# Kernel optimization log

Measured on AMD Instinct MI355X. Metric: run time of the kernel, lower is better.

The kernel has to match this reference:

```python
import jax, jax.numpy as jnp
import numpy as np

N_FILTRATIONS = 24
TEMPERATURE = 0.15
H1_WEIGHT = 0.5
LAMBDA_TOPO = 0.1


def setup_inputs() -> dict:
    key = jax.random.key(0)
    embeddings = jax.random.normal(key, (4096, 512), dtype=jnp.float32)
    return {"embeddings": embeddings, "step": 0}


def _landscape_loss(embeddings):
    N = embeddings.shape[0]
    emb = embeddings.astype(jnp.float32)
    # pairwise euclidean distances (torch.cdist p=2), safe sqrt for grad at 0
    sq = jnp.sum(emb * emb, axis=1)
    d2 = sq[:, None] + sq[None, :] - 2.0 * (emb @ emb.T)
    d2 = jnp.maximum(d2, 0.0)
    pos = d2 > 1e-12
    dist = jnp.where(pos, jnp.sqrt(jnp.where(pos, d2, 1.0)), 0.0)
    eye = jnp.eye(N, dtype=jnp.float32)
    dist = dist + eye * 1e9  # [N, N], diag pushed to 'infinity'
    off = dist < 1e8
    # thresholds come from .item() in torch -> no grad through them
    d_min = jax.lax.stop_gradient(jnp.min(jnp.where(off, dist, jnp.inf)))
    d_max = jax.lax.stop_gradient(
        jnp.maximum(jnp.max(jnp.where(off, dist, -jnp.inf)), d_min + 1e-4))
    thresholds = jnp.linspace(d_min, d_max, N_FILTRATIONS)

    one_minus_eye = 1.0 - eye

    def step_fn(carry, thresh):
        adj = jax.nn.sigmoid((thresh - dist) / TEMPERATURE) * one_minus_eye
        deg = jnp.clip(jnp.sum(adj, axis=-1), 1e-6, None)
        n_isolated = jnp.sum((deg < 0.5).astype(jnp.float32))  # H0 proxy
        n_edges_soft = jnp.sum(adj) / 2.0
        n_excess = jax.nn.relu(n_edges_soft - (N - 1)) / N  # H1 proxy
        return carry, (n_isolated, n_excess)

    _, (h0, h1) = jax.lax.scan(step_fn, None, thresholds)
    h0_loss = jnp.mean(h0[-8:])
    h1_loss = jnp.mean(h1)
    total = h0_loss + H1_WEIGHT * h1_loss
    return total * LAMBDA_TOPO


def reference(embeddings, step) -> jnp.ndarray:
    # warmup_steps = 0, so the warmup skip branch never triggers;
    # N == max_points, so no subsampling.
    return _landscape_loss(embeddings)
```

## Files before the change

kernel.cpp:

```cpp
#include <hip/hip_runtime.h>
#include <stdint.h>

typedef float f32x4 __attribute__((ext_vector_type(4)));
typedef short s16x8 __attribute__((ext_vector_type(8)));
typedef unsigned short us4 __attribute__((ext_vector_type(4)));

#define NPTS 4096
#define DDIM 512
#define NF   24
#define NBLK 32
#define NB   2048

#define OFF_SQ  4194304
#define OFF_MM  4210688
#define OFF_DEG 4210752
#define OFF_D   4603968
#define OFF_H   38158400ULL
#define WS_A    54935616ULL

static __device__ __forceinline__ ushort f2h(float x) {
    _Float16 h = (_Float16)x;
    return __builtin_bit_cast(unsigned short, h);
}
static __device__ __forceinline__ float h2f(ushort u) {
    return (float)__builtin_bit_cast(_Float16, u);
}

__global__ __launch_bounds__(256) void k_init(float* __restrict__ deg,
                                              unsigned* __restrict__ mm) {
    int i = blockIdx.x * 256 + threadIdx.x;
    if (i < NPTS * NF) deg[i] = 0.0f;
    if (i == 0) { mm[0] = 0x7F7FFFFFu; mm[1] = 0u; }
}

__global__ __launch_bounds__(256) void k_convert(const float* __restrict__ in,
                                                 ushort* __restrict__ Eb,
                                                 float* __restrict__ sq) {
    const int w = threadIdx.x >> 6, lane = threadIdx.x & 63;
    const int row = blockIdx.x * 4 + w;
    const float* src = in + (size_t)row * DDIM + lane * 8;
    float4 a = ((const float4*)src)[0];
    float4 b = ((const float4*)src)[1];
    float v[8] = {a.x, a.y, a.z, a.w, b.x, b.y, b.z, b.w};
    unsigned u[8];
    float ss = 0.0f;
#pragma unroll
    for (int i = 0; i < 8; ++i) {
        ss += v[i] * v[i];
        unsigned bits = __float_as_uint(v[i]);
        u[i] = (bits + 0x7FFFu + ((bits >> 16) & 1u)) >> 16;
    }
    uint4 pk;
    pk.x = u[0] | (u[1] << 16);
    pk.y = u[2] | (u[3] << 16);
    pk.z = u[4] | (u[5] << 16);
    pk.w = u[6] | (u[7] << 16);
    *(uint4*)(Eb + (size_t)row * DDIM + lane * 8) = pk;
#pragma unroll
    for (int s = 1; s < 64; s <<= 1) ss += __shfl_xor(ss, s);
    if (lane == 0) sq[row] = ss;
}

__global__ __launch_bounds__(256) void k_gram128T(const ushort* __restrict__ Eb,
                                                  const float* __restrict__ sq,
                                                  unsigned* __restrict__ mm,
                                                  ushort* __restrict__ D2h) {
    __shared__ ushort SM[4 * 128 * 40];
    __shared__ float sqr[128], sqc[128], red[8];
    const int tid = threadIdx.x;
    const int w = tid >> 6, lane = tid & 63, g = lane >> 4, l15 = lane & 15;

    int bid = blockIdx.x, rb = 0, pre = 0;
    while (pre + (NBLK - rb) <= bid) { pre += NBLK - rb; ++rb; }
    const int cb = rb + (bid - pre);

    if (tid < 128) sqr[tid] = sq[rb * 128 + tid];
    else           sqc[tid - 128] = sq[cb * 128 + (tid - 128)];

    f32x4 acc[2][8];
#pragma unroll
    for (int bi = 0; bi < 2; ++bi)
#pragma unroll
        for (int bj = 0; bj < 8; ++bj) acc[bi][bj] = (f32x4){0.f, 0.f, 0.f, 0.f};

    const int srow0 = tid >> 2, srow1 = 64 + (tid >> 2), sch = tid & 3;
    const size_t aoff0 = (size_t)(rb * 128 + srow0) * DDIM + sch * 8;
    const size_t aoff1 = (size_t)(rb * 128 + srow1) * DDIM + sch * 8;
    const size_t boff0 = (size_t)(cb * 128 + srow0) * DDIM + sch * 8;
    const size_t boff1 = (size_t)(cb * 128 + srow1) * DDIM + sch * 8;

    uint4 ra0 = *(const uint4*)(Eb + aoff0);
    uint4 ra1 = *(const uint4*)(Eb + aoff1);
    uint4 qb0 = *(const uint4*)(Eb + boff0);
    uint4 qb1 = *(const uint4*)(Eb + boff1);
    {
        ushort* A0 = SM;             ushort* B0 = SM + 2 * 5120;
        *(uint4*)(A0 + srow0 * 40 + sch * 8) = ra0;
        *(uint4*)(A0 + srow1 * 40 + sch * 8) = ra1;
        *(uint4*)(B0 + srow0 * 40 + sch * 8) = qb0;
        *(uint4*)(B0 + srow1 * 40 + sch * 8) = qb1;
    }
    int cur = 0;
#pragma unroll 1
    for (int kk = 0; kk < 16; ++kk) {
        if (kk < 15) {
            const int k1 = (kk + 1) * 32;
            ra0 = *(const uint4*)(Eb + aoff0 + k1);
            ra1 = *(const uint4*)(Eb + aoff1 + k1);
            qb0 = *(const uint4*)(Eb + boff0 + k1);
            qb1 = *(const uint4*)(Eb + boff1 + k1);
        }
        __syncthreads();
        const ushort* Ac = SM + cur * 5120;
        const ushort* Bc = SM + 2 * 5120 + cur * 5120;
        s16x8 rf0 = *(const s16x8*)(Ac + (w * 32 + l15) * 40 + g * 8);
        s16x8 rf1 = *(const s16x8*)(Ac + (w * 32 + 16 + l15) * 40 + g * 8);
#pragma unroll
        for (int bj = 0; bj < 8; ++bj) {
            s16x8 cf = *(const s16x8*)(Bc + (bj * 16 + l15) * 40 + g * 8);
            acc[0][bj] = __builtin_amdgcn_mfma_f32_16x16x32_bf16(cf, rf0, acc[0][bj], 0, 0, 0);
            acc[1][bj] = __builtin_amdgcn_mfma_f32_16x16x32_bf16(cf, rf1, acc[1][bj], 0, 0, 0);
        }
        if (kk < 15) {
            ushort* An = SM + (cur ^ 1) * 5120;
            ushort* Bn = SM + 2 * 5120 + (cur ^ 1) * 5120;
            *(uint4*)(An + srow0 * 40 + sch * 8) = ra0;
            *(uint4*)(An + srow1 * 40 + sch * 8) = ra1;
            *(uint4*)(Bn + srow0 * 40 + sch * 8) = qb0;
            *(uint4*)(Bn + srow1 * 40 + sch * 8) = qb1;
        }
        cur ^= 1;
    }
    __syncthreads();

    ushort* T = SM;
    float mn = 3.4e38f, mx = 0.0f;
#pragma unroll
    for (int bi = 0; bi < 2; ++bi) {
        const int trow = rb * 128 + w * 32 + bi * 16 + l15;
        const float srv = sqr[w * 32 + bi * 16 + l15];
#pragma unroll
        for (int bj = 0; bj < 8; ++bj) {
            const int c0 = bj * 16 + g * 4;
            const int tc0 = cb * 128 + c0;
            ushort h[4];
#pragma unroll
            for (int m = 0; m < 4; ++m) {
                float d2 = srv + sqc[c0 + m] - 2.0f * acc[bi][bj][m];
                d2 = fmaxf(d2, 0.0f);
                bool diag = (tc0 + m == trow);
                mn = diag ? mn : fminf(mn, d2);
                mx = diag ? mx : fmaxf(mx, d2);
                h[m] = f2h(diag ? 6.0e4f : d2);
            }
            us4 pk4 = {h[0], h[1], h[2], h[3]};
            *(us4*)(T + (w * 32 + bi * 16 + l15) * 136 + c0) = pk4;
        }
    }
#pragma unroll
    for (int s = 1; s < 64; s <<= 1) {
        mn = fminf(mn, __shfl_xor(mn, s));
        mx = fmaxf(mx, __shfl_xor(mx, s));
    }
    if (lane == 0) { red[w] = mn; red[4 + w] = mx; }
    __syncthreads();
    if (tid == 0) {
        mn = fminf(fminf(red[0], red[1]), fminf(red[2], red[3]));
        mx = fmaxf(fmaxf(red[4], red[5]), fmaxf(red[6], red[7]));
        atomicMin(&mm[0], __float_as_uint(mn));
        atomicMax(&mm[1], __float_as_uint(mx));
    }
    const int orow = tid >> 1, oh = tid & 1;
#pragma unroll
    for (int j = 0; j < 8; ++j) {
        uint4 v = *(const uint4*)(T + orow * 136 + oh * 64 + j * 8);
        *(uint4*)(D2h + (size_t)(rb * 128 + orow) * NPTS + cb * 128 + oh * 64 + j * 8) = v;
    }
    if (rb != cb) {
        const int ocol = tid >> 1;
#pragma unroll
        for (int j2 = 0; j2 < 8; ++j2) {
            unsigned pw[4];
#pragma unroll
            for (int p = 0; p < 4; ++p) {
                unsigned lo = T[(oh * 64 + j2 * 8 + 2 * p) * 136 + ocol];
                unsigned hi = T[(oh * 64 + j2 * 8 + 2 * p + 1) * 136 + ocol];
                pw[p] = lo | (hi << 16);
            }
            *(uint4*)(D2h + (size_t)(cb * 128 + ocol) * NPTS + rb * 128 + oh * 64 + j2 * 8) =
                *(uint4*)pw;
        }
    }
}

__global__ __launch_bounds__(256) void k_hist(const ushort* __restrict__ D2h,
                                              const unsigned* __restrict__ mm,
                                              ushort* __restrict__ H) {
    __shared__ unsigned hist[NB];
    const int tid = threadIdx.x;
    const int row = blockIdx.x;
    for (int i = tid; i < NB; i += 256) hist[i] = 0u;
    const float d2min = __uint_as_float(mm[0]);
    const float d2max = __uint_as_float(mm[1]);
    const float sc = (float)NB / fmaxf(d2max - d2min, 1e-6f);
    __syncthreads();
    const uint4* Dv = (const uint4*)(D2h + (size_t)row * NPTS);
#pragma unroll
    for (int c = 0; c < 2; ++c) {
        uint4 pk = Dv[c * 256 + tid];
        unsigned pw[4] = {pk.x, pk.y, pk.z, pk.w};
#pragma unroll
        for (int i = 0; i < 4; ++i) {
            float a = h2f((ushort)(pw[i] & 0xFFFFu));
            float b = h2f((ushort)(pw[i] >> 16));
            if (a < 3.0e4f) {
                int ba = (int)fminf(fmaxf((a - d2min) * sc, 0.0f), (float)(NB - 1));
                atomicAdd(&hist[ba], 1u);
            }
            if (b < 3.0e4f) {
                int bb = (int)fminf(fmaxf((b - d2min) * sc, 0.0f), (float)(NB - 1));
                atomicAdd(&hist[bb], 1u);
            }
        }
    }
    __syncthreads();
    unsigned o[4];
#pragma unroll
    for (int p = 0; p < 4; ++p) {
        unsigned lo = hist[tid * 8 + 2 * p], hi = hist[tid * 8 + 2 * p + 1];
        o[p] = (lo & 0xFFFFu) | (hi << 16);
    }
    *(uint4*)(H + (size_t)row * NB + tid * 8) = *(uint4*)o;
}

__global__ __launch_bounds__(512) void k_dot(const ushort* __restrict__ H,
                                             const unsigned* __restrict__ mm,
                                             float* __restrict__ deg) {
    __shared__ float Wl[4][NB];
    const int tid = threadIdx.x;
    const int wid = tid >> 6, lane = tid & 63;
    const int row = blockIdx.x * 8 + wid;

    const float d2min = __uint_as_float(mm[0]);
    const float d2max = __uint_as_float(mm[1]);
    const float bw    = fmaxf(d2max - d2min, 1e-6f) / (float)NB;
    const float d_min = d2min > 1e-12f ? sqrtf(d2min) : 0.0f;
    const float d_mx  = d2max > 1e-12f ? sqrtf(d2max) : 0.0f;
    const float d_max = fmaxf(d_mx, d_min + 1e-4f);
    const float stp   = (d_max - d_min) / 23.0f;
    const float S2L   = (1.0f / 0.15f) * 1.44269504f;
    const float Ds2   = stp * S2L;
    const float R     = exp2f(-Ds2);
    const float LIM   = 1073741824.0f;

    float hv[32];
    const ushort* Hr = H + (size_t)row * NB;
#pragma unroll
    for (int j = 0; j < 8; ++j) {
        uint2 pk = *(const uint2*)(Hr + j * 256 + lane * 4);
        hv[j * 4 + 0] = (float)(pk.x & 0xFFFFu);
        hv[j * 4 + 1] = (float)(pk.x >> 16);
        hv[j * 4 + 2] = (float)(pk.y & 0xFFFFu);
        hv[j * 4 + 3] = (float)(pk.y >> 16);
    }

    float e4[4];
#pragma unroll
    for (int q = 0; q < 4; ++q) {
        const int b = tid * 4 + q;
        const float d2c = d2min + ((float)b + 0.5f) * bw;
        const float db = sqrtf(fmaxf(d2c, 0.0f));
        e4[q] = exp2f(fminf((db - d_min) * S2L, 125.0f));
    }

#pragma unroll 1
    for (int ph = 0; ph < 6; ++ph) {
        __syncthreads();
#pragma unroll
        for (int k = 0; k < 4; ++k) {
            f32x4 sg;
#pragma unroll
            for (int q = 0; q < 4; ++q) {
                sg[q] = __builtin_amdgcn_rcpf(1.0f + fminf(e4[q], LIM));
                e4[q] *= R;
            }
            *(f32x4*)(&Wl[k][tid * 4]) = sg;
        }
        __syncthreads();
        float dacc[4];
#pragma unroll
        for (int k = 0; k < 4; ++k) {
            const float* Wr = &Wl[k][0];
            float s = 0.0f;
#pragma unroll
            for (int j = 0; j < 8; ++j) {
                const f32x4 wv = *(const f32x4*)(Wr + j * 256 + lane * 4);
                s += hv[j*4+0]*wv[0] + hv[j*4+1]*wv[1] + hv[j*4+2]*wv[2] + hv[j*4+3]*wv[3];
            }
            dacc[k] = s;
        }
#pragma unroll
        for (int k = 0; k < 4; ++k)
#pragma unroll
            for (int o = 1; o < 64; o <<= 1) dacc[k] += __shfl_xor(dacc[k], o);
        if (lane == 0) {
#pragma unroll
            for (int k = 0; k < 4; ++k) deg[(size_t)row * NF + ph * 4 + k] = dacc[k];
        }
    }
}

__device__ __forceinline__ void gram_tile(const ushort* __restrict__ Eb, int rb, int cb,
                                          ushort* As, ushort* Bs, f32x4 acc[2][8]) {
    const int tid = threadIdx.x;
    const int w = tid >> 6, lane = tid & 63, g = lane >> 4, l15 = lane & 15;
#pragma unroll 1
    for (int kk = 0; kk < DDIM / 32; ++kk) {
        const int k0 = kk * 32;
        __syncthreads();
#pragma unroll
        for (int it = 0; it < 2; ++it) {
            int li  = it * 256 + tid;
            int row = li >> 2, ch = li & 3;
            uint4 va = *(const uint4*)(Eb + (size_t)(rb * 128 + row) * DDIM + k0 + ch * 8);
            uint4 vb = *(const uint4*)(Eb + (size_t)(cb * 128 + row) * DDIM + k0 + ch * 8);
            *(uint4*)(As + row * 32 + ch * 8) = va;
            *(uint4*)(Bs + row * 32 + ch * 8) = vb;
        }
        __syncthreads();
        s16x8 rf0 = *(const s16x8*)(As + (w * 32 + 0 * 16 + l15) * 32 + g * 8);
        s16x8 rf1 = *(const s16x8*)(As + (w * 32 + 1 * 16 + l15) * 32 + g * 8);
#pragma unroll
        for (int bj = 0; bj < 8; ++bj) {
            s16x8 cf = *(const s16x8*)(Bs + (bj * 16 + l15) * 32 + g * 8);
            acc[0][bj] = __builtin_amdgcn_mfma_f32_16x16x32_bf16(cf, rf0, acc[0][bj], 0, 0, 0);
            acc[1][bj] = __builtin_amdgcn_mfma_f32_16x16x32_bf16(cf, rf1, acc[1][bj], 0, 0, 0);
        }
    }
}

__global__ __launch_bounds__(256) void k_minmax(const ushort* __restrict__ Eb,
                                                const float* __restrict__ sq,
                                                unsigned* __restrict__ mm) {
    const int rb = blockIdx.y, cb = blockIdx.x;
    if (cb < rb) return;
    __shared__ ushort As[128 * 32], Bs[128 * 32];
    __shared__ float sqr[128], sqc[128];
    __shared__ float red[8];
    const int tid = threadIdx.x;
    if (tid < 128) sqr[tid] = sq[rb * 128 + tid];
    else           sqc[tid - 128] = sq[cb * 128 + (tid - 128)];
    f32x4 acc[2][8];
#pragma unroll
    for (int bi = 0; bi < 2; ++bi)
#pragma unroll
        for (int bj = 0; bj < 8; ++bj) acc[bi][bj] = (f32x4){0.f, 0.f, 0.f, 0.f};
    gram_tile(Eb, rb, cb, As, Bs, acc);
    const int w = tid >> 6, lane = tid & 63, g = lane >> 4, l15 = lane & 15;
    const float sr0 = sqr[w * 32 + l15], sr1 = sqr[w * 32 + 16 + l15];
    float mn = 3.4e38f, mx = 0.0f;
#pragma unroll
    for (int bi = 0; bi < 2; ++bi)
#pragma unroll
        for (int bj = 0; bj < 8; ++bj)
#pragma unroll
            for (int m = 0; m < 4; ++m) {
                int tr = w * 32 + bi * 16 + l15;
                int tc = bj * 16 + g * 4 + m;
                float d2 = (bi ? sr1 : sr0) + sqc[tc] - 2.0f * acc[bi][bj][m];
                d2 = fmaxf(d2, 0.0f);
                bool diag = (rb == cb) && (tr == tc);
                mn = diag ? mn : fminf(mn, d2);
                mx = diag ? mx : fmaxf(mx, d2);
            }
#pragma unroll
    for (int s = 1; s < 64; s <<= 1) {
        mn = fminf(mn, __shfl_xor(mn, s));
        mx = fmaxf(mx, __shfl_xor(mx, s));
    }
    if (lane == 0) { red[w] = mn; red[4 + w] = mx; }
    __syncthreads();
    if (tid == 0) {
        mn = fminf(fminf(red[0], red[1]), fminf(red[2], red[3]));
        mx = fmaxf(fmaxf(red[4], red[5]), fmaxf(red[6], red[7]));
        atomicMin(&mm[0], __float_as_uint(mn));
        atomicMax(&mm[1], __float_as_uint(mx));
    }
}

__global__ __launch_bounds__(256) void k_accum2(const ushort* __restrict__ Eb,
                                                const float* __restrict__ sq,
                                                const unsigned* __restrict__ mm,
                                                float* __restrict__ deg) {
    const int rb = blockIdx.y, cb = blockIdx.x;
    __shared__ ushort As[128 * 32], Bs[128 * 32];
    __shared__ float sqr[128], sqc[128];
    __shared__ float degr[128][NF];
    const int tid = threadIdx.x;
    if (tid < 128) sqr[tid] = sq[rb * 128 + tid];
    else           sqc[tid - 128] = sq[cb * 128 + (tid - 128)];
    for (int i = tid; i < 128 * NF; i += 256) ((float*)degr)[i] = 0.0f;
    f32x4 acc[2][8];
#pragma unroll
    for (int bi = 0; bi < 2; ++bi)
#pragma unroll
        for (int bj = 0; bj < 8; ++bj) acc[bi][bj] = (f32x4){0.f, 0.f, 0.f, 0.f};
    gram_tile(Eb, rb, cb, As, Bs, acc);
    const int w = tid >> 6, lane = tid & 63, g = lane >> 4, l15 = lane & 15;

    const float dmin2 = __uint_as_float(mm[0]);
    const float dmax2 = __uint_as_float(mm[1]);
    const float d_min = dmin2 > 1e-12f ? sqrtf(dmin2) : 0.0f;
    const float d_mx  = dmax2 > 1e-12f ? sqrtf(dmax2) : 0.0f;
    const float d_max = fmaxf(d_mx, d_min + 1e-4f);
    const float stp   = (d_max - d_min) / 23.0f;
    const float S2L   = (1.0f / 0.15f) * 1.44269504f;
    const float Ds2   = stp * S2L;
    const float R     = exp2f(-Ds2);
    const float LIM   = 1073741824.0f;
    const float ECAP  = 125.0f;

    const float sr0 = sqr[w * 32 + l15], sr1 = sqr[w * 32 + 16 + l15];
    f32x4 ee[2][8];
#pragma unroll
    for (int bi = 0; bi < 2; ++bi)
#pragma unroll
        for (int bj = 0; bj < 8; ++bj)
#pragma unroll
            for (int m = 0; m < 4; ++m) {
                int tr = w * 32 + bi * 16 + l15;
                int tc = bj * 16 + g * 4 + m;
                float d2 = (bi ? sr1 : sr0) + sqc[tc] - 2.0f * acc[bi][bj][m];
                d2 = fmaxf(d2, 0.0f);
                float d = d2 > 1e-12f ? sqrtf(d2) : 0.0f;
                if (rb == cb && tr == tc) d = 1e9f;
                ee[bi][bj][m] = exp2f(fminf((d - d_min) * S2L, ECAP));
            }

#pragma unroll 1
    for (int t = 0; t < NF; ++t) {
        float rs0 = 0.0f, rs1 = 0.0f;
#pragma unroll
        for (int bj = 0; bj < 8; ++bj) {
            {
                f32x4 q = ee[0][bj];
                float A  = 1.0f + fminf(q.x, LIM), B  = 1.0f + fminf(q.y, LIM);
                float Cq = 1.0f + fminf(q.z, LIM), Dq = 1.0f + fminf(q.w, LIM);
                float sAB = A + B,  sCD = Cq + Dq;
                float pAB = A * B,  pCD = Cq * Dq;
                rs0 += (sAB * pCD + sCD * pAB) * __builtin_amdgcn_rcpf(pAB * pCD);
                ee[0][bj] = q * R;
            }
            {
                f32x4 q = ee[1][bj];
                float A  = 1.0f + fminf(q.x, LIM), B  = 1.0f + fminf(q.y, LIM);
                float Cq = 1.0f + fminf(q.z, LIM), Dq = 1.0f + fminf(q.w, LIM);
                float sAB = A + B,  sCD = Cq + Dq;
                float pAB = A * B,  pCD = Cq * Dq;
                rs1 += (sAB * pCD + sCD * pAB) * __builtin_amdgcn_rcpf(pAB * pCD);
                ee[1][bj] = q * R;
            }
        }
        rs0 += __shfl_xor(rs0, 16); rs0 += __shfl_xor(rs0, 32);
        rs1 += __shfl_xor(rs1, 16); rs1 += __shfl_xor(rs1, 32);
        if (g == 0) {
            degr[w * 32 + l15][t]      += rs0;
            degr[w * 32 + 16 + l15][t] += rs1;
        }
    }
    __syncthreads();
    for (int i = tid; i < 128 * NF; i += 256) {
        int r = i / NF, t = i % NF;
        atomicAdd(&deg[(size_t)(rb * 128 + r) * NF + t], degr[r][t]);
    }
}

__global__ __launch_bounds__(256) void k_final(const float* __restrict__ deg,
                                               float* __restrict__ out) {
    const int tid = threadIdx.x;
    float s[NF], cnt[8];
#pragma unroll
    for (int t = 0; t < NF; ++t) s[t] = 0.0f;
#pragma unroll
    for (int k = 0; k < 8; ++k) cnt[k] = 0.0f;
    for (int i = tid; i < NPTS; i += 256) {
        const float* row = deg + (size_t)i * NF;
#pragma unroll
        for (int t = 0; t < NF; ++t) {
            float v = row[t];
            s[t] += v;
            if (t >= 16) cnt[t - 16] += (v < 0.5f) ? 1.0f : 0.0f;
        }
    }
#pragma unroll
    for (int t = 0; t < NF; ++t)
#pragma unroll
        for (int o = 1; o < 64; o <<= 1) s[t] += __shfl_xor(s[t], o);
#pragma unroll
    for (int k = 0; k < 8; ++k)
#pragma unroll
        for (int o = 1; o < 64; o <<= 1) cnt[k] += __shfl_xor(cnt[k], o);
    __shared__ float red[4][32];
    const int w = tid >> 6, lane = tid & 63;
    if (lane == 0) {
#pragma unroll
        for (int t = 0; t < NF; ++t) red[w][t] = s[t];
#pragma unroll
        for (int k = 0; k < 8; ++k) red[w][NF + k] = cnt[k];
    }
    __syncthreads();
    if (tid == 0) {
        float h0 = 0.0f, h1 = 0.0f;
#pragma unroll
        for (int t = 0; t < NF; ++t) {
            float S = red[0][t] + red[1][t] + red[2][t] + red[3][t];
            float edges = S * 0.5f;
            h1 += fmaxf(edges - (float)(NPTS - 1), 0.0f) / (float)NPTS;
        }
#pragma unroll
        for (int k = 0; k < 8; ++k)
            h0 += red[0][NF + k] + red[1][NF + k] + red[2][NF + k] + red[3][NF + k];
        h0 *= (1.0f / 8.0f);
        h1 *= (1.0f / 24.0f);
        out[0] = (h0 + 0.5f * h1) * 0.1f;
    }
}

extern "C" void kernel_launch(void* const* d_in, const int* in_sizes, int n_in,
                              void* d_out, int out_size, void* d_ws, size_t ws_size,
                              hipStream_t stream) {
    (void)in_sizes; (void)n_in; (void)out_size;
    const float* emb = (const float*)d_in[0];
    uint8_t* ws = (uint8_t*)d_ws;
    ushort*   Eb  = (ushort*)(ws);
    float*    sqv = (float*)(ws + OFF_SQ);
    unsigned* mm  = (unsigned*)(ws + OFF_MM);
    float*    deg = (float*)(ws + OFF_DEG);
    ushort*   D2h = (ushort*)(ws + OFF_D);
    ushort*   H   = (ushort*)(ws + OFF_H);
    float*    out = (float*)d_out;
    const bool bigws = (ws_size >= WS_A);

    k_init   <<<dim3(384),      dim3(256), 0, stream>>>(deg, mm);
    k_convert<<<dim3(NPTS / 4), dim3(256), 0, stream>>>(emb, Eb, sqv);
    if (bigws) {
        k_gram128T<<<dim3(NBLK * (NBLK + 1) / 2), dim3(256), 0, stream>>>(Eb, sqv, mm, D2h);
        k_hist    <<<dim3(NPTS),                  dim3(256), 0, stream>>>(D2h, mm, H);
        k_dot     <<<dim3(NPTS / 8),              dim3(512), 0, stream>>>(H, mm, deg);
    } else {
        k_minmax<<<dim3(32, 32), dim3(256), 0, stream>>>(Eb, sqv, mm);
        k_accum2<<<dim3(32, 32), dim3(256), 0, stream>>>(Eb, sqv, mm, deg);
    }
    k_final<<<1, 256, 0, stream>>>(deg, out);
}
```

Measured before the change: 92.42 us.

## Compute full Gram grid with 2x2 warp tiling and fuse degree reduction into k_dot

The symmetric upper-triangle Gram kernel with a transposed write-back is replaced by a full 32x32 block grid, remapped so neighbouring blocks spread across the grid. Each warp now computes a 64x64 sub-tile through a 2x2 warp arrangement, which improves fragment reuse. The uncoalesced transposed stores go away, at the cost of doing twice the MFMA work. k_dot now reduces degrees per block and atomically accumulates the edge sums and isolated counts into a small buffer, so a lighter final kernel replaces the per-row degree array read.

Result: slower. 96.93 us (+4.9%).

```diff
diff --git a/kernel.cpp b/kernel.cpp
--- a/kernel.cpp
+++ b/kernel.cpp
@@ -61,27 +61,27 @@
     if (lane == 0) sq[row] = ss;
 }
 
-__global__ __launch_bounds__(256) void k_gram128T(const ushort* __restrict__ Eb,
-                                                  const float* __restrict__ sq,
-                                                  unsigned* __restrict__ mm,
-                                                  ushort* __restrict__ D2h) {
+__global__ __launch_bounds__(256) void k_gram_full(const ushort* __restrict__ Eb,
+                                                   const float* __restrict__ sq,
+                                                   unsigned* __restrict__ mm,
+                                                   ushort* __restrict__ D2h) {
     __shared__ ushort SM[4 * 128 * 40];
     __shared__ float sqr[128], sqc[128], red[8];
     const int tid = threadIdx.x;
     const int w = tid >> 6, lane = tid & 63, g = lane >> 4, l15 = lane & 15;
-
-    int bid = blockIdx.x, rb = 0, pre = 0;
-    while (pre + (NBLK - rb) <= bid) { pre += NBLK - rb; ++rb; }
-    const int cb = rb + (bid - pre);
+    const int wr = w >> 1, wc = w & 1;
+
+    const int bid = (blockIdx.x & 7) * 128 + (blockIdx.x >> 3);
+    const int rb = bid >> 5, cb = bid & 31;
 
     if (tid < 128) sqr[tid] = sq[rb * 128 + tid];
     else           sqc[tid - 128] = sq[cb * 128 + (tid - 128)];
 
-    f32x4 acc[2][8];
-#pragma unroll
-    for (int bi = 0; bi < 2; ++bi)
-#pragma unroll
-        for (int bj = 0; bj < 8; ++bj) acc[bi][bj] = (f32x4){0.f, 0.f, 0.f, 0.f};
+    f32x4 acc[4][4];
+#pragma unroll
+    for (int i = 0; i < 4; ++i)
+#pragma unroll
+        for (int j = 0; j < 4; ++j) acc[i][j] = (f32x4){0.f, 0.f, 0.f, 0.f};
 
     const int srow0 = tid >> 2, srow1 = 64 + (tid >> 2), sch = tid & 3;
     const size_t aoff0 = (size_t)(rb * 128 + srow0) * DDIM + sch * 8;
@@ -113,14 +113,18 @@
         __syncthreads();
         const ushort* Ac = SM + cur * 5120;
         const ushort* Bc = SM + 2 * 5120 + cur * 5120;
-        s16x8 rf0 = *(const s16x8*)(Ac + (w * 32 + l15) * 40 + g * 8);
-        s16x8 rf1 = *(const s16x8*)(Ac + (w * 32 + 16 + l15) * 40 + g * 8);
-#pragma unroll
-        for (int bj = 0; bj < 8; ++bj) {
-            s16x8 cf = *(const s16x8*)(Bc + (bj * 16 + l15) * 40 + g * 8);
-            acc[0][bj] = __builtin_amdgcn_mfma_f32_16x16x32_bf16(cf, rf0, acc[0][bj], 0, 0, 0);
-            acc[1][bj] = __builtin_amdgcn_mfma_f32_16x16x32_bf16(cf, rf1, acc[1][bj], 0, 0, 0);
-        }
+        s16x8 rf[4], cf[4];
+#pragma unroll
+        for (int i = 0; i < 4; ++i)
+            rf[i] = *(const s16x8*)(Ac + (wr * 64 + i * 16 + l15) * 40 + g * 8);
+#pragma unroll
+        for (int j = 0; j < 4; ++j)
+            cf[j] = *(const s16x8*)(Bc + (wc * 64 + j * 16 + l15) * 40 + g * 8);
+#pragma unroll
+        for (int i = 0; i < 4; ++i)
+#pragma unroll
+            for (int j = 0; j < 4; ++j)
+                acc[i][j] = __builtin_amdgcn_mfma_f32_16x16x32_bf16(cf[j], rf[i], acc[i][j], 0, 0, 0);
         if (kk < 15) {
             ushort* An = SM + (cur ^ 1) * 5120;
             ushort* Bn = SM + 2 * 5120 + (cur ^ 1) * 5120;
@@ -136,17 +140,18 @@
     ushort* T = SM;
     float mn = 3.4e38f, mx = 0.0f;
 #pragma unroll
-    for (int bi = 0; bi < 2; ++bi) {
-        const int trow = rb * 128 + w * 32 + bi * 16 + l15;
-        const float srv = sqr[w * 32 + bi * 16 + l15];
-#pragma unroll
-        for (int bj = 0; bj < 8; ++bj) {
-            const int c0 = bj * 16 + g * 4;
+    for (int i = 0; i < 4; ++i) {
+        const int lrow = wr * 64 + i * 16 + l15;
+        const int trow = rb * 128 + lrow;
+        const float srv = sqr[lrow];
+#pragma unroll
+        for (int j = 0; j < 4; ++j) {
+            const int c0 = wc * 64 + j * 16 + g * 4;
             const int tc0 = cb * 128 + c0;
             ushort h[4];
 #pragma unroll
             for (int m = 0; m < 4; ++m) {
-                float d2 = srv + sqc[c0 + m] - 2.0f * acc[bi][bj][m];
+                float d2 = srv + sqc[c0 + m] - 2.0f * acc[i][j][m];
                 d2 = fmaxf(d2, 0.0f);
                 bool diag = (tc0 + m == trow);
                 mn = diag ? mn : fminf(mn, d2);
@@ -154,7 +159,7 @@
                 h[m] = f2h(diag ? 6.0e4f : d2);
             }
             us4 pk4 = {h[0], h[1], h[2], h[3]};
-            *(us4*)(T + (w * 32 + bi * 16 + l15) * 136 + c0) = pk4;
+            *(us4*)(T + lrow * 136 + c0) = pk4;
         }
     }
 #pragma unroll
@@ -175,21 +180,6 @@
     for (int j = 0; j < 8; ++j) {
         uint4 v = *(const uint4*)(T + orow * 136 + oh * 64 + j * 8);
         *(uint4*)(D2h + (size_t)(rb * 128 + orow) * NPTS + cb * 128 + oh * 64 + j * 8) = v;
-    }
-    if (rb != cb) {
-        const int ocol = tid >> 1;
-#pragma unroll
-        for (int j2 = 0; j2 < 8; ++j2) {
-            unsigned pw[4];
-#pragma unroll
-            for (int p = 0; p < 4; ++p) {
-                unsigned lo = T[(oh * 64 + j2 * 8 + 2 * p) * 136 + ocol];
-                unsigned hi = T[(oh * 64 + j2 * 8 + 2 * p + 1) * 136 + ocol];
-                pw[p] = lo | (hi << 16);
-            }
-            *(uint4*)(D2h + (size_t)(cb * 128 + ocol) * NPTS + rb * 128 + oh * 64 + j2 * 8) =
-                *(uint4*)pw;
-        }
     }
 }
 
@@ -235,8 +225,9 @@
 
 __global__ __launch_bounds__(512) void k_dot(const ushort* __restrict__ H,
                                              const unsigned* __restrict__ mm,
-                                             float* __restrict__ deg) {
+                                             float* __restrict__ acc32) {
     __shared__ float Wl[4][NB];
+    __shared__ float degb[8][NF];
     const int tid = threadIdx.x;
     const int wid = tid >> 6, lane = tid & 63;
     const int row = blockIdx.x * 8 + wid;
@@ -305,8 +296,35 @@
             for (int o = 1; o < 64; o <<= 1) dacc[k] += __shfl_xor(dacc[k], o);
         if (lane == 0) {
 #pragma unroll
-            for (int k = 0; k < 4; ++k) deg[(size_t)row * NF + ph * 4 + k] = dacc[k];
-        }
+            for (int k = 0; k < 4; ++k) degb[wid][ph * 4 + k] = dacc[k];
+        }
+    }
+    __syncthreads();
+    if (tid < NF) {
+        float s = 0.0f;
+#pragma unroll
+        for (int r = 0; r < 8; ++r) s += degb[r][tid];
+        atomicAdd(&acc32[tid], s);
+    } else if (tid < 32) {
+        const int k = 16 + (tid - NF);
+        float c = 0.0f;
+#pragma unroll
+        for (int r = 0; r < 8; ++r) c += (degb[r][k] < 0.5f) ? 1.0f : 0.0f;
+        atomicAdd(&acc32[tid], c);
+    }
+}
+
+__global__ __launch_bounds__(64) void k_final2(const float* __restrict__ acc32,
+                                               float* __restrict__ out) {
+    if (threadIdx.x == 0) {
+        float h1 = 0.0f;
+#pragma unroll
+        for (int k = 0; k < NF; ++k)
+            h1 += fmaxf(acc32[k] * 0.5f - (float)(NPTS - 1), 0.0f) * (1.0f / (float)NPTS);
+        float h0 = 0.0f;
+#pragma unroll
+        for (int k = 0; k < 8; ++k) h0 += acc32[NF + k];
+        out[0] = (h0 * 0.125f + 0.5f * (h1 * (1.0f / 24.0f))) * 0.1f;
     }
 }
 
@@ -544,12 +562,13 @@
     k_init   <<<dim3(384),      dim3(256), 0, stream>>>(deg, mm);
     k_convert<<<dim3(NPTS / 4), dim3(256), 0, stream>>>(emb, Eb, sqv);
     if (bigws) {
-        k_gram128T<<<dim3(NBLK * (NBLK + 1) / 2), dim3(256), 0, stream>>>(Eb, sqv, mm, D2h);
-        k_hist    <<<dim3(NPTS),                  dim3(256), 0, stream>>>(D2h, mm, H);
-        k_dot     <<<dim3(NPTS / 8),              dim3(512), 0, stream>>>(H, mm, deg);
+        k_gram_full<<<dim3(NBLK * NBLK), dim3(256), 0, stream>>>(Eb, sqv, mm, D2h);
+        k_hist     <<<dim3(NPTS),        dim3(256), 0, stream>>>(D2h, mm, H);
+        k_dot      <<<dim3(NPTS / 8),    dim3(512), 0, stream>>>(H, mm, deg);
+        k_final2   <<<dim3(1),           dim3(64),  0, stream>>>(deg, out);
     } else {
         k_minmax<<<dim3(32, 32), dim3(256), 0, stream>>>(Eb, sqv, mm);
         k_accum2<<<dim3(32, 32), dim3(256), 0, stream>>>(Eb, sqv, mm, deg);
-    }
-    k_final<<<1, 256, 0, stream>>>(deg, out);
-}
+        k_final <<<dim3(1),      dim3(256), 0, stream>>>(deg, out);
+    }
+}
```
